# Kernel optimization log

Hardware: AMD Instinct MI355X
Metric: run time of the kernel (lower is better)

Reference implementation:

```python
import math
import jax, jax.numpy as jnp
import numpy as np

B, S, E, H = 1, 2048, 2048, 16
QL, KL = 1536, 512          # q_lora_rank, kv_lora_rank
DN, DR, DV = 128, 64, 128   # qk_nope_head_dim, qk_rope_head_dim, v_head_dim
DQ = DN + DR                # q_head_dim = 192
ROPE_BASE = 10000.0
EPS = 1e-6


def _rope_cache(seq_len):
    # YaRN with scaling_factor=1.0 reduces exactly to standard RoPE (freq_extra == freq_inter,
    # mscale ratio == 1), matching DeepseekV2YarnRotaryEmbedding at default settings.
    inv_freq = 1.0 / (ROPE_BASE ** (np.arange(0, DR, 2, dtype=np.float32) / DR))
    t = np.arange(seq_len, dtype=np.float32)
    freqs = np.outer(t, inv_freq)
    emb = np.concatenate([freqs, freqs], axis=-1)  # (S, DR)
    return jnp.asarray(np.cos(emb)), jnp.asarray(np.sin(emb))


def _rmsnorm(x, w):
    return x * jax.lax.rsqrt(jnp.mean(x * x, axis=-1, keepdims=True) + EPS) * w


def _apply_rope(x, cos, sin):
    # x: (B, S, H, D). DeepseekV2 apply_rotary_pos_emb first de-interleaves
    # (view(..., d//2, 2).transpose) then uses rotate_half.
    b, s, h, d = x.shape
    xr = x.reshape(b, s, h, d // 2, 2)
    x = jnp.concatenate([xr[..., 0], xr[..., 1]], axis=-1)  # de-interleave
    rot = jnp.concatenate([-x[..., d // 2:], x[..., : d // 2]], axis=-1)
    return x * cos[None, :, None, :] + rot * sin[None, :, None, :]


def setup_inputs() -> dict:
    key = jax.random.key(0)
    ks = jax.random.split(key, 8)
    w = lambda k, shape, fan_in: (jax.random.normal(k, shape, jnp.float32) / math.sqrt(fan_in))
    return {
        "x": jax.random.normal(ks[0], (B, S, E), jnp.float32),
        "w_q_a": w(ks[1], (E, QL), E),
        "q_a_ln": jnp.ones((QL,), jnp.float32),
        "w_q_b": w(ks[2], (QL, H * DQ), QL),
        "w_kv_a": w(ks[3], (E, KL + DR), E),
        "kv_a_ln": jnp.ones((KL,), jnp.float32),
        "w_kv_b": w(ks[4], (KL, H * (DN + DV)), KL),
        "w_out": w(ks[5], (H * DV, E), H * DV),
    }


def reference(x, w_q_a, q_a_ln, w_q_b, w_kv_a, kv_a_ln, w_kv_b, w_out):
    b, s, _ = x.shape
    # Q: low-rank down-proj -> RMSNorm -> up-proj, split nope/rope parts
    q = (_rmsnorm(x @ w_q_a, q_a_ln) @ w_q_b).reshape(b, s, H, DQ)
    q_nope, q_pe = q[..., :DN], q[..., DN:]
    # KV: joint compressed latent + shared (MQA-style) rope key
    ckv = x @ w_kv_a                         # (b, s, KL+DR)
    c_kv, k_pe = ckv[..., :KL], ckv[..., KL:]
    kv = (_rmsnorm(c_kv, kv_a_ln) @ w_kv_b).reshape(b, s, H, DN + DV)
    k_nope, v = kv[..., :DN], kv[..., DN:]
    # Partial RoPE on the 64-dim rope slice only
    cos, sin = _rope_cache(s)
    q_pe = _apply_rope(q_pe, cos, sin)
    k_pe = _apply_rope(k_pe.reshape(b, s, 1, DR), cos, sin)
    qf = jnp.concatenate([q_nope, q_pe], axis=-1)                       # (b,s,H,192)
    kf = jnp.concatenate([k_nope, jnp.broadcast_to(k_pe, (b, s, H, DR))], axis=-1)
    # Causal softmax attention, scale = 1/sqrt(q_head_dim)
    scale = 1.0 / math.sqrt(DQ)
    scores = jnp.einsum("bqhd,bkhd->bhqk", qf, kf) * scale
    mask = jnp.tril(jnp.ones((s, s), dtype=bool))
    scores = jnp.where(mask[None, None], scores, jnp.finfo(scores.dtype).min)
    p = jax.nn.softmax(scores, axis=-1)
    o = jnp.einsum("bhqk,bkhd->bqhd", p, v).reshape(b, s, H * DV)
    return o @ w_out
```

## Files before the change

### kernel.cpp

```cpp
#include <hip/hip_runtime.h>
#include <hip/hip_bf16.h>
#include <math.h>

#define SS   2048
#define EE   2048
#define HH   16
#define QLAT 1536
#define KLAT 512
#define DN   128
#define DR   64
#define DV   128
#define DQ   192
#define KVD  256
#define CKVW 576
#define QW   3072
#define KVW  4096
#define OW   2048
#define QAC  2112

#define NSEG 4
#define PT_STRIDE 72
#define KTSZ (6 * 64 * 32)

typedef __attribute__((ext_vector_type(8))) short short8;
typedef __attribute__((ext_vector_type(4))) float f32x4;

__global__ void detect_dtype(const unsigned int* __restrict__ lnw, int* flag) {
    *flag = (lnw[0] == 0x3F803F80u) ? 1 : 0;
}

__device__ __forceinline__ float ld_in(const void* p, size_t i, int bf) {
    if (bf) return __bfloat162float(((const __hip_bfloat16*)p)[i]);
    return ((const float*)p)[i];
}

__device__ __forceinline__ ushort f2b(float v) {
    __hip_bfloat16 b = __float2bfloat16(v);
    return *(ushort*)&b;
}
__device__ __forceinline__ float b2f(ushort u) {
    __hip_bfloat16 b = *(__hip_bfloat16*)&u;
    return __bfloat162float(b);
}

__device__ __forceinline__ void async16(const ushort* g, ushort* l) {
    __builtin_amdgcn_global_load_lds(
        (const __attribute__((address_space(1))) void*)g,
        (__attribute__((address_space(3))) void*)l, 16, 0, 0);
}

__global__ __launch_bounds__(256) void conv_x_bf(
    const void* __restrict__ src, ushort* __restrict__ dst, int n, const int* flag) {
    const int bf = *flag;
    int i = (blockIdx.x * 256 + threadIdx.x) * 4;
    if (i >= n) return;
    ushort4 u;
    u.x = f2b(ld_in(src, i + 0, bf));
    u.y = f2b(ld_in(src, i + 1, bf));
    u.z = f2b(ld_in(src, i + 2, bf));
    u.w = f2b(ld_in(src, i + 3, bf));
    *(ushort4*)(dst + i) = u;
}

__global__ __launch_bounds__(256) void transpose5_bf(
    const void* __restrict__ s0, const void* __restrict__ s1,
    const void* __restrict__ s2, const void* __restrict__ s3,
    const void* __restrict__ s4,
    ushort* __restrict__ d0, ushort* __restrict__ d1, ushort* __restrict__ d2,
    ushort* __restrict__ d3, ushort* __restrict__ d4,
    const int* flag) {
    const int z = blockIdx.z;
    const void* in; ushort* out; int R, C;
    switch (z) {
        case 0:  in = s0; out = d0; R = EE;   C = QLAT; break;
        case 1:  in = s1; out = d1; R = EE;   C = CKVW; break;
        case 2:  in = s2; out = d2; R = QLAT; C = QW;   break;
        case 3:  in = s3; out = d3; R = KLAT; C = KVW;  break;
        default: in = s4; out = d4; R = OW;   C = EE;   break;
    }
    const int c0 = blockIdx.x * 64, r0 = blockIdx.y * 64;
    if (c0 >= C || r0 >= R) return;
    const int bf = *flag;
    __shared__ ushort t[64][66];
    const int lane = threadIdx.x & 63, grp = threadIdx.x >> 6;
    #pragma unroll
    for (int p = 0; p < 16; ++p) {
        int r = p * 4 + grp;
        t[lane][r] = f2b(ld_in(in, (size_t)(r0 + r) * C + c0 + lane, bf));
    }
    __syncthreads();
    const int ro = (threadIdx.x & 31) * 2, co = threadIdx.x >> 5;
    #pragma unroll
    for (int p = 0; p < 8; ++p) {
        int c = p * 8 + co;
        ushort2 u = *(const ushort2*)&t[c][ro];
        *(ushort2*)&out[(size_t)(c0 + c) * R + r0 + ro] = u;
    }
}

__device__ __forceinline__ void gemm128_body(
    const ushort* __restrict__ A, const ushort* __restrict__ Bt,
    void* __restrict__ C, int N, int K, int lda, int ldb, int ldc,
    int cbf, int bm, int bn, ushort* As, ushort* Bs) {
    const int tid = threadIdx.x;
    const int lane = tid & 63, wv = tid >> 6;
    const int wm = (wv & 1) * 64, wn = (wv >> 1) * 64;
    const int ln = lane & 15, quad = lane >> 4;

    f32x4 acc[4][4];
    #pragma unroll
    for (int i = 0; i < 4; ++i)
        #pragma unroll
        for (int j = 0; j < 4; ++j) acc[i][j] = (f32x4){0.f, 0.f, 0.f, 0.f};

    const int srow = tid >> 3;
    const int spart = ((tid & 7) ^ ((tid >> 3) & 7)) * 8;
    const ushort* Ag0 = A + (size_t)(bm + srow) * lda + spart;
    const ushort* Ag1 = Ag0 + (size_t)32 * lda;
    const ushort* Ag2 = Ag0 + (size_t)64 * lda;
    const ushort* Ag3 = Ag0 + (size_t)96 * lda;
    const int br0 = (bn + srow)      < N ? (bn + srow)      : (N - 1);
    const int br1 = (bn + 32 + srow) < N ? (bn + 32 + srow) : (N - 1);
    const int br2 = (bn + 64 + srow) < N ? (bn + 64 + srow) : (N - 1);
    const int br3 = (bn + 96 + srow) < N ? (bn + 96 + srow) : (N - 1);
    const ushort* Bg0 = Bt + (size_t)br0 * ldb + spart;
    const ushort* Bg1 = Bt + (size_t)br1 * ldb + spart;
    const ushort* Bg2 = Bt + (size_t)br2 * ldb + spart;
    const ushort* Bg3 = Bt + (size_t)br3 * ldb + spart;
    const int nsteps = K >> 6;

    {
        ushort* as = As + tid * 8;
        ushort* bs = Bs + tid * 8;
        async16(Ag0, as);          async16(Ag1, as + 2048);
        async16(Ag2, as + 4096);   async16(Ag3, as + 6144);
        async16(Bg0, bs);          async16(Bg1, bs + 2048);
        async16(Bg2, bs + 4096);   async16(Bg3, bs + 6144);
    }

    int cb = 0;
    for (int c = 0; c < nsteps; ++c) {
        asm volatile("s_waitcnt vmcnt(0)" ::: "memory");
        __builtin_amdgcn_s_barrier();
        asm volatile("" ::: "memory");
        if (c + 1 < nsteps) {
            const int k1 = (c + 1) << 6;
            ushort* as = As + (cb ^ 1) * 8192 + tid * 8;
            ushort* bs = Bs + (cb ^ 1) * 8192 + tid * 8;
            async16(Ag0 + k1, as);          async16(Ag1 + k1, as + 2048);
            async16(Ag2 + k1, as + 4096);   async16(Ag3 + k1, as + 6144);
            async16(Bg0 + k1, bs);          async16(Bg1 + k1, bs + 2048);
            async16(Bg2 + k1, bs + 4096);   async16(Bg3 + k1, bs + 6144);
        }
        const ushort* Ac = As + cb * 8192;
        const ushort* Bc = Bs + cb * 8192;
        #pragma unroll
        for (int ks = 0; ks < 2; ++ks) {
            const int sw = ((ks * 4 + quad) ^ (ln & 7)) * 8;
            short8 af[4], bfr[4];
            #pragma unroll
            for (int t = 0; t < 4; ++t) {
                af[t]  = *(const short8*)&Ac[(wm + t * 16 + ln) * 64 + sw];
                bfr[t] = *(const short8*)&Bc[(wn + t * 16 + ln) * 64 + sw];
            }
            __builtin_amdgcn_s_setprio(1);
            #pragma unroll
            for (int i = 0; i < 4; ++i)
                #pragma unroll
                for (int j = 0; j < 4; ++j)
                    acc[i][j] = __builtin_amdgcn_mfma_f32_16x16x32_bf16(af[i], bfr[j], acc[i][j], 0, 0, 0);
            __builtin_amdgcn_s_setprio(0);
        }
        cb ^= 1;
    }

    #pragma unroll
    for (int i = 0; i < 4; ++i) {
        #pragma unroll
        for (int r = 0; r < 4; ++r) {
            const int m = bm + wm + i * 16 + quad * 4 + r;
            #pragma unroll
            for (int j = 0; j < 4; ++j) {
                const int n = bn + wn + j * 16 + ln;
                if (n < N) {
                    if (cbf) ((ushort*)C)[(size_t)m * ldc + n] = f2b(acc[i][j][r]);
                    else     ((float*)C)[(size_t)m * ldc + n] = acc[i][j][r];
                }
            }
        }
    }
}

__global__ __launch_bounds__(256) void gemm_qkv(
    const ushort* __restrict__ qac, const ushort* __restrict__ wqbt,
    const ushort* __restrict__ wkvbt, ushort* __restrict__ qbf_,
    ushort* __restrict__ kvbf_) {
    __shared__ ushort As[2 * 8192];
    __shared__ ushort Bs[2 * 8192];
    if (blockIdx.z == 0) {
        if (blockIdx.x >= QW / 128) return;
        gemm128_body(qac, wqbt, qbf_, QW, QLAT, QAC, QLAT, QW, 1,
                     blockIdx.y * 128, blockIdx.x * 128, As, Bs);
    } else {
        gemm128_body(qac + QLAT, wkvbt, kvbf_, KVW, KLAT, QAC, KLAT, KVW, 1,
                     blockIdx.y * 128, blockIdx.x * 128, As, Bs);
    }
}

__global__ __launch_bounds__(256) void gemm_bf64(
    const ushort* __restrict__ A, const ushort* __restrict__ Bt,
    void* __restrict__ C, int N, int K, int lda, int ldb, int ldc,
    int cmode, const int* __restrict__ cflag) {
    __shared__ ushort As[2 * 4096];
    __shared__ ushort Bs[2 * 8192];
    const int tid = threadIdx.x;
    const int bm = blockIdx.y * 64, bn = blockIdx.x * 128;
    const int lane = tid & 63, wv = tid >> 6;
    const int wm = (wv & 1) * 32, wn = (wv >> 1) * 64;
    const int ln = lane & 15, quad = lane >> 4;

    int cbf = cmode;
    if (cmode == 2) cbf = *(volatile const int*)cflag;

    f32x4 acc[2][4];
    #pragma unroll
    for (int i = 0; i < 2; ++i)
        #pragma unroll
        for (int j = 0; j < 4; ++j) acc[i][j] = (f32x4){0.f, 0.f, 0.f, 0.f};

    const int srow = tid >> 3;
    const int spart = ((tid & 7) ^ ((tid >> 3) & 7)) * 8;
    const ushort* Ag0 = A + (size_t)(bm + srow) * lda + spart;
    const ushort* Ag1 = Ag0 + (size_t)32 * lda;
    const int br0 = (bn + srow)      < N ? (bn + srow)      : (N - 1);
    const int br1 = (bn + 32 + srow) < N ? (bn + 32 + srow) : (N - 1);
    const int br2 = (bn + 64 + srow) < N ? (bn + 64 + srow) : (N - 1);
    const int br3 = (bn + 96 + srow) < N ? (bn + 96 + srow) : (N - 1);
    const ushort* Bg0 = Bt + (size_t)br0 * ldb + spart;
    const ushort* Bg1 = Bt + (size_t)br1 * ldb + spart;
    const ushort* Bg2 = Bt + (size_t)br2 * ldb + spart;
    const ushort* Bg3 = Bt + (size_t)br3 * ldb + spart;
    const int nsteps = K >> 6;

    {
        ushort* as = As + tid * 8;
        ushort* bs = Bs + tid * 8;
        async16(Ag0, as);          async16(Ag1, as + 2048);
        async16(Bg0, bs);          async16(Bg1, bs + 2048);
        async16(Bg2, bs + 4096);   async16(Bg3, bs + 6144);
    }

    int cb = 0;
    for (int c = 0; c < nsteps; ++c) {
        asm volatile("s_waitcnt vmcnt(0)" ::: "memory");
        __builtin_amdgcn_s_barrier();
        asm volatile("" ::: "memory");
        if (c + 1 < nsteps) {
            const int k1 = (c + 1) << 6;
            ushort* as = As + (cb ^ 1) * 4096 + tid * 8;
            ushort* bs = Bs + (cb ^ 1) * 8192 + tid * 8;
            async16(Ag0 + k1, as);          async16(Ag1 + k1, as + 2048);
            async16(Bg0 + k1, bs);          async16(Bg1 + k1, bs + 2048);
            async16(Bg2 + k1, bs + 4096);   async16(Bg3 + k1, bs + 6144);
        }
        const ushort* Ac = As + cb * 4096;
        const ushort* Bc = Bs + cb * 8192;
        #pragma unroll
        for (int ks = 0; ks < 2; ++ks) {
            const int sw = ((ks * 4 + quad) ^ (ln & 7)) * 8;
            short8 af[2], bfr[4];
            #pragma unroll
            for (int t = 0; t < 2; ++t)
                af[t] = *(const short8*)&Ac[(wm + t * 16 + ln) * 64 + sw];
            #pragma unroll
            for (int t = 0; t < 4; ++t)
                bfr[t] = *(const short8*)&Bc[(wn + t * 16 + ln) * 64 + sw];
            __builtin_amdgcn_s_setprio(1);
            #pragma unroll
            for (int i = 0; i < 2; ++i)
                #pragma unroll
                for (int j = 0; j < 4; ++j)
                    acc[i][j] = __builtin_amdgcn_mfma_f32_16x16x32_bf16(af[i], bfr[j], acc[i][j], 0, 0, 0);
            __builtin_amdgcn_s_setprio(0);
        }
        cb ^= 1;
    }

    #pragma unroll
    for (int i = 0; i < 2; ++i) {
        #pragma unroll
        for (int r = 0; r < 4; ++r) {
            const int m = bm + wm + i * 16 + quad * 4 + r;
            #pragma unroll
            for (int j = 0; j < 4; ++j) {
                const int n = bn + wn + j * 16 + ln;
                if (n < N) {
                    if (cbf) ((ushort*)C)[(size_t)m * ldc + n] = f2b(acc[i][j][r]);
                    else     ((float*)C)[(size_t)m * ldc + n] = acc[i][j][r];
                }
            }
        }
    }
}

__global__ __launch_bounds__(256) void rmsnorm2_bf(
    ushort* __restrict__ x, const void* __restrict__ wq,
    const void* __restrict__ wkv, const int* wflag) {
    const int wbf = *wflag;
    const int which = blockIdx.y;
    const int cols = which ? KLAT : QLAT;
    const void* w = which ? wkv : wq;
    ushort* p = x + (size_t)blockIdx.x * QAC + (which ? QLAT : 0);
    float ss = 0.f;
    for (int i = threadIdx.x; i < cols; i += 256) { float v = b2f(p[i]); ss += v * v; }
    #pragma unroll
    for (int off = 32; off; off >>= 1) ss += __shfl_xor(ss, off);
    __shared__ float red[4];
    const int wid = threadIdx.x >> 6, lane = threadIdx.x & 63;
    if (lane == 0) red[wid] = ss;
    __syncthreads();
    const float tot = red[0] + red[1] + red[2] + red[3];
    const float scale = rsqrtf(tot / (float)cols + 1e-6f);
    for (int i = threadIdx.x; i < cols; i += 256)
        p[i] = f2b(b2f(p[i]) * scale * ld_in(w, i, wbf));
}

__global__ __launch_bounds__(256) void rope_tab(float* __restrict__ tab) {
    int idx = blockIdx.x * 256 + threadIdx.x;
    int s = idx >> 5, i = idx & 31;
    float inv = powf(10000.0f, -(float)i / 32.0f);
    float sv, cv;
    sincosf((float)s * inv, &sv, &cv);
    tab[idx * 2]     = cv;
    tab[idx * 2 + 1] = sv;
}

__device__ __forceinline__ void rope_block(
    const ushort* __restrict__ src, ushort* __restrict__ dst,
    const float* __restrict__ tb) {
    short8 vin[8];
    #pragma unroll
    for (int t = 0; t < 8; ++t) vin[t] = *(const short8*)(src + t * 8);
    short8 lo[4], hi[4];
    #pragma unroll
    for (int t = 0; t < 4; ++t) {
        #pragma unroll
        for (int j = 0; j < 8; ++j) {
            const int i = t * 8 + j;
            float cv = tb[2 * i], sv = tb[2 * i + 1];
            ushort u0 = ((const ushort*)&vin[(2 * i) >> 3])[(2 * i) & 7];
            ushort u1 = ((const ushort*)&vin[(2 * i + 1) >> 3])[(2 * i + 1) & 7];
            float x0 = b2f(u0), x1 = b2f(u1);
            lo[t][j] = (short)f2b(x0 * cv - x1 * sv);
            hi[t][j] = (short)f2b(x1 * cv + x0 * sv);
        }
    }
    #pragma unroll
    for (int t = 0; t < 4; ++t) {
        *(short8*)(dst + t * 8)      = lo[t];
        *(short8*)(dst + 32 + t * 8) = hi[t];
    }
}

__global__ __launch_bounds__(256) void fuse3(
    ushort* __restrict__ q, const ushort* __restrict__ qac,
    const ushort* __restrict__ kv, ushort* __restrict__ kf,
    ushort* __restrict__ vt2, const float* __restrict__ tab) {
    __shared__ ushort Vl[64 * 136];
    const int b = blockIdx.x;
    const int tid = threadIdx.x;
    if (b < 128) {
        int idx = b * 256 + tid;
        int s = idx >> 4, h = idx & 15;
        ushort* p = q + (size_t)s * QW + h * DQ + DN;
        rope_block(p, p, tab + s * 64);
    } else if (b < 128 + 3072) {
        int idx = (b - 128) * 256 + tid;
        int part = idx % 24;
        int rest = idx / 24;
        int h = rest & 15, s = rest >> 4;
        short8 v;
        if (part < 16) {
            v = *(const short8*)(kv + (size_t)s * KVW + h * KVD + part * 8);
        } else {
            const int j8 = part - 16;
            const int seg = j8 & 3;
            const ushort* cp = qac + (size_t)s * QAC + QLAT + KLAT + seg * 16;
            short8 a = *(const short8*)cp;
            short8 bb = *(const short8*)(cp + 8);
            const float* tb = tab + s * 64 + seg * 16;
            const bool hi = (j8 >= 4);
            #pragma unroll
            for (int jj = 0; jj < 8; ++jj) {
                float cv = tb[2 * jj], sv = tb[2 * jj + 1];
                ushort u0 = (jj < 4) ? (ushort)a[2 * jj]     : (ushort)bb[2 * jj - 8];
                ushort u1 = (jj < 4) ? (ushort)a[2 * jj + 1] : (ushort)bb[2 * jj - 7];
                float x0 = b2f(u0), x1 = b2f(u1);
                v[jj] = (short)f2b(hi ? (x1 * cv + x0 * sv) : (x0 * cv - x1 * sv));
            }
        }
        *(short8*)(kf + ((size_t)h * SS + s) * 192 + part * 8) = v;
    } else {
        const int r = b - (128 + 3072);
        const int ck = r & 31, h = r >> 5;
        const int lane = tid & 63, wv = tid >> 6;
        #pragma unroll
        for (int rr = 0; rr < 4; ++rr) {
            int n = rr * 256 + tid;
            int key = n >> 4, part = n & 15;
            short8 v = *(const short8*)(kv + (size_t)(ck * 64 + key) * KVW + h * KVD + DN + part * 8);
            *(short8*)&Vl[key * 136 + part * 8] = v;
        }
        __syncthreads();
        const int ln = lane & 15, quad = lane >> 4;
        ushort* dst = vt2 + (((size_t)h * 32 + ck) * 16) * 512;
        #pragma unroll
        for (int w = 0; w < 4; ++w) {
            int idx2 = wv * 4 + w;
            int kb2 = idx2 >> 3, nb = idx2 & 7;
            short8 v;
            #pragma unroll
            for (int j = 0; j < 8; ++j)
                ((ushort*)&v)[j] = Vl[(kb2 * 32 + quad * 8 + j) * 136 + nb * 16 + ln];
            *(short8*)(dst + (size_t)idx2 * 512 + lane * 8) = v;
        }
    }
}

__global__ __launch_bounds__(256, 2) void attn_mfma2(
    const ushort* __restrict__ qbf, const ushort* __restrict__ kf,
    const ushort* __restrict__ vt2, ushort* __restrict__ opart,
    float* __restrict__ ml) {
    const int seg = blockIdx.x, bq = 31 - blockIdx.y, h = blockIdx.z;
    const int ctot = bq + 1;
    const int c_lo = (seg * ctot) >> 2;
    const int nch = (((seg + 1) * ctot) >> 2) - c_lo;
    if (nch <= 0) return;

    __shared__ ushort Kt[2 * KTSZ];
    __shared__ ushort Pt[4][16 * PT_STRIDE];

    const int tid = threadIdx.x, lane = tid & 63, wl = tid >> 6;
    const int ln = lane & 15, quad = lane >> 4;
    const int qw = bq * 64 + wl * 16;
    const int kstart = c_lo << 6;
    const float scale = 0.07216878364870322f;

    short8 aq[6];
    const ushort* qrow = qbf + (size_t)(qw + ln) * QW + h * DQ;
    #pragma unroll
    for (int kb = 0; kb < 6; ++kb)
        aq[kb] = *(const short8*)(qrow + kb * 32 + quad * 8);

    const ushort* kfh = kf + (size_t)h * SS * 192;
    const ushort* vth2 = vt2 + ((size_t)h * 32 * 16) * 512 + lane * 8;

    const int key_s = tid >> 2;
    const int swp = ((tid & 3) ^ ((tid >> 3) & 3)) * 8;
    const ushort* kg = kfh + (size_t)(kstart + key_s) * 192 + swp;
    const int swq = (quad ^ ((ln >> 1) & 3)) * 8;

    f32x4 oacc[8];
    #pragma unroll
    for (int f = 0; f < 8; ++f) oacc[f] = (f32x4){0.f, 0.f, 0.f, 0.f};
    float mrow[4] = {-INFINITY, -INFINITY, -INFINITY, -INFINITY};
    float lrow[4] = {0.f, 0.f, 0.f, 0.f};

    {
        ushort* kd = Kt + tid * 8;
        #pragma unroll
        for (int i = 0; i < 6; ++i)
            async16(kg + i * 32, kd + i * 2048);
        kg += (size_t)64 * 192;
    }

    for (int c = 0; c < nch; ++c) {
        const int k0 = kstart + (c << 6);
        asm volatile("s_waitcnt vmcnt(0)" ::: "memory");
        __builtin_amdgcn_s_barrier();
        asm volatile("" ::: "memory");
        if (c + 1 < nch) {
            ushort* kd = Kt + ((c + 1) & 1) * KTSZ + tid * 8;
            #pragma unroll
            for (int i = 0; i < 6; ++i)
                async16(kg + i * 32, kd + i * 2048);
            kg += (size_t)64 * 192;
        }
        const ushort* Kcur = Kt + (c & 1) * KTSZ;

        const ushort* vfr = vth2 + (size_t)(k0 >> 6) * 16 * 512;
        short8 bv0[8];
        #pragma unroll
        for (int nb = 0; nb < 8; ++nb)
            bv0[nb] = *(const short8*)(vfr + (size_t)nb * 512);
        f32x4 s[4];
        #pragma unroll
        for (int ns = 0; ns < 4; ++ns) s[ns] = (f32x4){0.f, 0.f, 0.f, 0.f};
        __builtin_amdgcn_s_setprio(1);
        #pragma unroll
        for (int ns = 0; ns < 4; ++ns)
            #pragma unroll
            for (int kb = 0; kb < 6; ++kb) {
                short8 bk = *(const short8*)&Kcur[(kb * 64 + ns * 16 + ln) * 32 + swq];
                s[ns] = __builtin_amdgcn_mfma_f32_16x16x32_bf16(aq[kb], bk, s[ns], 0, 0, 0);
            }
        __builtin_amdgcn_s_setprio(0);
        float pv[4][4], rmax[4];
        #pragma unroll
        for (int r = 0; r < 4; ++r) rmax[r] = -1e30f;
        #pragma unroll
        for (int ns = 0; ns < 4; ++ns)
            #pragma unroll
            for (int r = 0; r < 4; ++r) {
                int key = k0 + ns * 16 + ln;
                int qr = qw + quad * 4 + r;
                float v = s[ns][r] * scale;
                if (key > qr) v = -1e30f;
                pv[ns][r] = v;
                rmax[r] = fmaxf(rmax[r], v);
            }
        #pragma unroll
        for (int off = 8; off; off >>= 1)
            #pragma unroll
            for (int r = 0; r < 4; ++r)
                rmax[r] = fmaxf(rmax[r], __shfl_xor(rmax[r], off));
        float alpha[4], psum[4];
        #pragma unroll
        for (int r = 0; r < 4; ++r) {
            float mnew = fmaxf(mrow[r], rmax[r]);
            alpha[r] = __expf(mrow[r] - mnew);
            mrow[r] = mnew;
        }
        #pragma unroll
        for (int ns = 0; ns < 4; ++ns)
            #pragma unroll
            for (int r = 0; r < 4; ++r)
                pv[ns][r] = __expf(pv[ns][r] - mrow[r]);
        #pragma unroll
        for (int r = 0; r < 4; ++r)
            psum[r] = (pv[0][r] + pv[1][r]) + (pv[2][r] + pv[3][r]);
        #pragma unroll
        for (int off = 8; off; off >>= 1)
            #pragma unroll
            for (int r = 0; r < 4; ++r)
                psum[r] += __shfl_xor(psum[r], off);
        #pragma unroll
        for (int r = 0; r < 4; ++r) lrow[r] = lrow[r] * alpha[r] + psum[r];
        #pragma unroll
        for (int f = 0; f < 8; ++f)
            #pragma unroll
            for (int r = 0; r < 4; ++r) oacc[f][r] *= alpha[r];
        #pragma unroll
        for (int ns = 0; ns < 4; ++ns)
            #pragma unroll
            for (int r = 0; r < 4; ++r)
                Pt[wl][(quad * 4 + r) * PT_STRIDE + ns * 16 + ln] = f2b(pv[ns][r]);
        short8 bv1[8];
        #pragma unroll
        for (int nb = 0; nb < 8; ++nb)
            bv1[nb] = *(const short8*)(vfr + (size_t)(8 + nb) * 512);
        short8 pa0 = *(const short8*)&Pt[wl][ln * PT_STRIDE + quad * 8];
        short8 pa1 = *(const short8*)&Pt[wl][ln * PT_STRIDE + 32 + quad * 8];
        __builtin_amdgcn_s_setprio(1);
        #pragma unroll
        for (int nb = 0; nb < 8; ++nb)
            oacc[nb] = __builtin_amdgcn_mfma_f32_16x16x32_bf16(pa0, bv0[nb], oacc[nb], 0, 0, 0);
        #pragma unroll
        for (int nb = 0; nb < 8; ++nb)
            oacc[nb] = __builtin_amdgcn_mfma_f32_16x16x32_bf16(pa1, bv1[nb], oacc[nb], 0, 0, 0);
        __builtin_amdgcn_s_setprio(0);
    }

    const size_t pbase = (((size_t)h * 32 + bq) * NSEG + seg) * 64;
    #pragma unroll
    for (int nb = 0; nb < 8; ++nb)
        #pragma unroll
        for (int r = 0; r < 4; ++r)
            opart[(pbase + wl * 16 + quad * 4 + r) * 128 + nb * 16 + ln] = f2b(oacc[nb][r]);
    if (ln == 0) {
        #pragma unroll
        for (int r = 0; r < 4; ++r) {
            ml[(pbase + wl * 16 + quad * 4 + r) * 2]     = mrow[r];
            ml[(pbase + wl * 16 + quad * 4 + r) * 2 + 1] = lrow[r];
        }
    }
}

__global__ __launch_bounds__(256) void merge_attn(
    const ushort* __restrict__ opart, const float* __restrict__ ml,
    ushort* __restrict__ obf) {
    const int q = blockIdx.x;
    const int bq = q >> 6, row = q & 63;
    const int ctot = bq + 1;
    const int t = threadIdx.x;
    #pragma unroll
    for (int pp = 0; pp < 8; ++pp) {
        int idx = pp * 256 + t;
        int h = idx >> 7, d = idx & 127;
        size_t rbase = (((size_t)h * 32 + bq) * NSEG) * 64 + row;
        float M = -1e30f;
        #pragma unroll
        for (int s = 0; s < NSEG; ++s) {
            if ((((s + 1) * ctot) >> 2) > ((s * ctot) >> 2))
                M = fmaxf(M, ml[(rbase + (size_t)s * 64) * 2]);
        }
        float L = 0.f, acc = 0.f;
        #pragma unroll
        for (int s = 0; s < NSEG; ++s) {
            if ((((s + 1) * ctot) >> 2) > ((s * ctot) >> 2)) {
                size_t ri = rbase + (size_t)s * 64;
                float w = __expf(ml[ri * 2] - M);
                L += w * ml[ri * 2 + 1];
                acc += w * b2f(opart[ri * 128 + d]);
            }
        }
        obf[(size_t)q * OW + h * DV + d] = f2b(acc / L);
    }
}

extern "C" void kernel_launch(void* const* d_in, const int* in_sizes, int n_in,
                              void* d_out, int out_size, void* d_ws, size_t ws_size,
                              hipStream_t stream) {
    const void* x       = d_in[0];
    const void* w_q_a   = d_in[1];
    const void* q_a_ln  = d_in[2];
    const void* w_q_b   = d_in[3];
    const void* w_kv_a  = d_in[4];
    const void* kv_a_ln = d_in[5];
    const void* w_kv_b  = d_in[6];
    const void* w_out   = d_in[7];

    char* ws = (char*)d_ws;
    int*    flag  = (int*)ws;
    ushort* qbf   = (ushort*)(ws + 256);
    ushort* obf   = qbf   + (size_t)SS * QW;
    ushort* wqat  = obf   + (size_t)SS * OW;
    ushort* wkvat = wqat  + (size_t)QLAT * EE;
    ushort* wqbt  = wkvat + (size_t)CKVW * EE;
    ushort* wkvbt = wqbt  + (size_t)QW * QLAT;
    ushort* woutt = wkvbt + (size_t)KVW * KLAT;
    ushort* kf    = woutt + (size_t)EE * OW;
    ushort* vt2   = kf    + (size_t)HH * SS * 192;
    float*  ml    = (float*)(vt2 + (size_t)HH * SS * DV);
    ushort* qac   = (ushort*)(ml + (size_t)HH * 32 * NSEG * 64 * 2);
    ushort* xbf   = qac   + (size_t)SS * QAC;
    ushort* kvbf  = xbf   + (size_t)SS * EE;
    ushort* kpebf = kvbf  + (size_t)SS * KVW;
    float*  rtab  = (float*)(kpebf + (size_t)SS * DR);
    ushort* opart = qac;

    detect_dtype<<<1, 1, 0, stream>>>((const unsigned int*)q_a_ln, flag);
    rope_tab<<<SS * 32 / 256, 256, 0, stream>>>(rtab);

    conv_x_bf<<<(SS * EE / 4 + 255) / 256, 256, 0, stream>>>(x, xbf, SS * EE, flag);
    transpose5_bf<<<dim3(64, 32, 5), 256, 0, stream>>>(
        w_q_a, w_kv_a, w_q_b, w_kv_b, w_out,
        wqat, wkvat, wqbt, wkvbt, woutt, flag);

    gemm_bf64<<<dim3((QAC + 127) / 128, SS / 64), 256, 0, stream>>>(
        xbf, wqat, qac, QAC, EE, EE, EE, QAC, 1, nullptr);

    rmsnorm2_bf<<<dim3(SS, 2), 256, 0, stream>>>(qac, q_a_ln, kv_a_ln, flag);

    gemm_qkv<<<dim3(KVW / 128, SS / 128, 2), 256, 0, stream>>>(
        qac, wqbt, wkvbt, qbf, kvbf);

    fuse3<<<128 + 3072 + 512, 256, 0, stream>>>(qbf, qac, kvbf, kf, vt2, rtab);

    attn_mfma2<<<dim3(NSEG, SS / 64, HH), 256, 0, stream>>>(qbf, kf, vt2, opart, ml);
    merge_attn<<<SS, 256, 0, stream>>>(opart, ml, obf);

    gemm_bf64<<<dim3(EE / 128, SS / 64), 256, 0, stream>>>(
        obf, woutt, d_out, EE, OW, OW, OW, EE, 2, flag);
}
```

Measured before the change: 372.2 us.

## Double query rows per attention block to reuse K/V tiles across two groups

Each attention workgroup now handles 128 query rows instead of 64, with each wave owning two 16-row groups that share the same K tile in LDS and the same V fragments. This halves K tile loads and block count per head. Fully masked chunks for a group are skipped, and the causal mask is applied only on diagonal chunks. The cost is higher register pressure from doubled accumulators and Q fragments, which may hurt occupancy with launch bounds of 2, plus fewer blocks to fill the GPU.

```diff
diff --git a/kernel.cpp b/kernel.cpp
--- a/kernel.cpp
+++ b/kernel.cpp
@@ -431,8 +431,8 @@
     const ushort* __restrict__ qbf, const ushort* __restrict__ kf,
     const ushort* __restrict__ vt2, ushort* __restrict__ opart,
     float* __restrict__ ml) {
-    const int seg = blockIdx.x, bq = 31 - blockIdx.y, h = blockIdx.z;
-    const int ctot = bq + 1;
+    const int seg = blockIdx.x, bq = 15 - blockIdx.y, h = blockIdx.z;
+    const int ctot = 2 * bq + 2;
     const int c_lo = (seg * ctot) >> 2;
     const int nch = (((seg + 1) * ctot) >> 2) - c_lo;
     if (nch <= 0) return;
@@ -442,15 +442,18 @@
 
     const int tid = threadIdx.x, lane = tid & 63, wl = tid >> 6;
     const int ln = lane & 15, quad = lane >> 4;
-    const int qw = bq * 64 + wl * 16;
+    const int qw = bq * 128 + wl * 32;
     const int kstart = c_lo << 6;
     const float scale = 0.07216878364870322f;
 
-    short8 aq[6];
-    const ushort* qrow = qbf + (size_t)(qw + ln) * QW + h * DQ;
-    #pragma unroll
-    for (int kb = 0; kb < 6; ++kb)
-        aq[kb] = *(const short8*)(qrow + kb * 32 + quad * 8);
+    short8 aq[2][6];
+    #pragma unroll
+    for (int g = 0; g < 2; ++g) {
+        const ushort* qrow = qbf + (size_t)(qw + g * 16 + ln) * QW + h * DQ;
+        #pragma unroll
+        for (int kb = 0; kb < 6; ++kb)
+            aq[g][kb] = *(const short8*)(qrow + kb * 32 + quad * 8);
+    }
 
     const ushort* kfh = kf + (size_t)h * SS * 192;
     const ushort* vth2 = vt2 + ((size_t)h * 32 * 16) * 512 + lane * 8;
@@ -460,11 +463,16 @@
     const ushort* kg = kfh + (size_t)(kstart + key_s) * 192 + swp;
     const int swq = (quad ^ ((ln >> 1) & 3)) * 8;
 
-    f32x4 oacc[8];
-    #pragma unroll
-    for (int f = 0; f < 8; ++f) oacc[f] = (f32x4){0.f, 0.f, 0.f, 0.f};
-    float mrow[4] = {-INFINITY, -INFINITY, -INFINITY, -INFINITY};
-    float lrow[4] = {0.f, 0.f, 0.f, 0.f};
+    f32x4 oacc[2][8];
+    #pragma unroll
+    for (int g = 0; g < 2; ++g)
+        #pragma unroll
+        for (int f = 0; f < 8; ++f) oacc[g][f] = (f32x4){0.f, 0.f, 0.f, 0.f};
+    float mrow[2][4], lrow[2][4];
+    #pragma unroll
+    for (int g = 0; g < 2; ++g)
+        #pragma unroll
+        for (int r = 0; r < 4; ++r) { mrow[g][r] = -INFINITY; lrow[g][r] = 0.f; }
 
     {
         ushort* kd = Kt + tid * 8;
@@ -487,101 +495,112 @@
             kg += (size_t)64 * 192;
         }
         const ushort* Kcur = Kt + (c & 1) * KTSZ;
-
         const ushort* vfr = vth2 + (size_t)(k0 >> 6) * 16 * 512;
-        short8 bv0[8];
+
+        #pragma unroll
+        for (int g = 0; g < 2; ++g) {
+            const int qg = qw + g * 16;
+            if (k0 > qg + 15) continue;
+            f32x4 s[4];
+            #pragma unroll
+            for (int ns = 0; ns < 4; ++ns) s[ns] = (f32x4){0.f, 0.f, 0.f, 0.f};
+            __builtin_amdgcn_s_setprio(1);
+            #pragma unroll
+            for (int ns = 0; ns < 4; ++ns)
+                #pragma unroll
+                for (int kb = 0; kb < 6; ++kb) {
+                    short8 bk = *(const short8*)&Kcur[(kb * 64 + ns * 16 + ln) * 32 + swq];
+                    s[ns] = __builtin_amdgcn_mfma_f32_16x16x32_bf16(aq[g][kb], bk, s[ns], 0, 0, 0);
+                }
+            __builtin_amdgcn_s_setprio(0);
+            float pv[4][4], rmax[4];
+            #pragma unroll
+            for (int ns = 0; ns < 4; ++ns)
+                #pragma unroll
+                for (int r = 0; r < 4; ++r)
+                    pv[ns][r] = s[ns][r] * scale;
+            if (k0 + 63 > qg) {
+                #pragma unroll
+                for (int ns = 0; ns < 4; ++ns)
+                    #pragma unroll
+                    for (int r = 0; r < 4; ++r)
+                        if (k0 + ns * 16 + ln > qg + quad * 4 + r) pv[ns][r] = -1e30f;
+            }
+            #pragma unroll
+            for (int r = 0; r < 4; ++r)
+                rmax[r] = fmaxf(fmaxf(pv[0][r], pv[1][r]), fmaxf(pv[2][r], pv[3][r]));
+            #pragma unroll
+            for (int off = 8; off; off >>= 1)
+                #pragma unroll
+                for (int r = 0; r < 4; ++r)
+                    rmax[r] = fmaxf(rmax[r], __shfl_xor(rmax[r], off));
+            float alpha[4], psum[4];
+            #pragma unroll
+            for (int r = 0; r < 4; ++r) {
+                float mnew = fmaxf(mrow[g][r], rmax[r]);
+                alpha[r] = __expf(mrow[g][r] - mnew);
+                mrow[g][r] = mnew;
+            }
+            #pragma unroll
+            for (int ns = 0; ns < 4; ++ns)
+                #pragma unroll
+                for (int r = 0; r < 4; ++r)
+                    pv[ns][r] = __expf(pv[ns][r] - mrow[g][r]);
+            #pragma unroll
+            for (int r = 0; r < 4; ++r)
+                psum[r] = (pv[0][r] + pv[1][r]) + (pv[2][r] + pv[3][r]);
+            #pragma unroll
+            for (int off = 8; off; off >>= 1)
+                #pragma unroll
+                for (int r = 0; r < 4; ++r)
+                    psum[r] += __shfl_xor(psum[r], off);
+            #pragma unroll
+            for (int r = 0; r < 4; ++r) lrow[g][r] = lrow[g][r] * alpha[r] + psum[r];
+            #pragma unroll
+            for (int f = 0; f < 8; ++f)
+                #pragma unroll
+                for (int r = 0; r < 4; ++r) oacc[g][f][r] *= alpha[r];
+            #pragma unroll
+            for (int ns = 0; ns < 4; ++ns)
+                #pragma unroll
+                for (int r = 0; r < 4; ++r)
+                    Pt[wl][(quad * 4 + r) * PT_STRIDE + ns * 16 + ln] = f2b(pv[ns][r]);
+            short8 bv0[8], bv1[8];
+            #pragma unroll
+            for (int nb = 0; nb < 8; ++nb) {
+                bv0[nb] = *(const short8*)(vfr + (size_t)nb * 512);
+                bv1[nb] = *(const short8*)(vfr + (size_t)(8 + nb) * 512);
+            }
+            short8 pa0 = *(const short8*)&Pt[wl][ln * PT_STRIDE + quad * 8];
+            short8 pa1 = *(const short8*)&Pt[wl][ln * PT_STRIDE + 32 + quad * 8];
+            __builtin_amdgcn_s_setprio(1);
+            #pragma unroll
+            for (int nb = 0; nb < 8; ++nb)
+                oacc[g][nb] = __builtin_amdgcn_mfma_f32_16x16x32_bf16(pa0, bv0[nb], oacc[g][nb], 0, 0, 0);
+            #pragma unroll
+            for (int nb = 0; nb < 8; ++nb)
+                oacc[g][nb] = __builtin_amdgcn_mfma_f32_16x16x32_bf16(pa1, bv1[nb], oacc[g][nb], 0, 0, 0);
+            __builtin_amdgcn_s_setprio(0);
+        }
+    }
+
+    const size_t pbase = (((size_t)h * 16 + bq) * NSEG + seg) * 128;
+    #pragma unroll
+    for (int g = 0; g < 2; ++g) {
         #pragma unroll
         for (int nb = 0; nb < 8; ++nb)
-            bv0[nb] = *(const short8*)(vfr + (size_t)nb * 512);
-        f32x4 s[4];
-        #pragma unroll
-        for (int ns = 0; ns < 4; ++ns) s[ns] = (f32x4){0.f, 0.f, 0.f, 0.f};
-        __builtin_amdgcn_s_setprio(1);
-        #pragma unroll
-        for (int ns = 0; ns < 4; ++ns)
-            #pragma unroll
-            for (int kb = 0; kb < 6; ++kb) {
-                short8 bk = *(const short8*)&Kcur[(kb * 64 + ns * 16 + ln) * 32 + swq];
-                s[ns] = __builtin_amdgcn_mfma_f32_16x16x32_bf16(aq[kb], bk, s[ns], 0, 0, 0);
-            }
-        __builtin_amdgcn_s_setprio(0);
-        float pv[4][4], rmax[4];
-        #pragma unroll
-        for (int r = 0; r < 4; ++r) rmax[r] = -1e30f;
-        #pragma unroll
-        for (int ns = 0; ns < 4; ++ns)
             #pragma unroll
             for (int r = 0; r < 4; ++r) {
-                int key = k0 + ns * 16 + ln;
-                int qr = qw + quad * 4 + r;
-                float v = s[ns][r] * scale;
-                if (key > qr) v = -1e30f;
-                pv[ns][r] = v;
-                rmax[r] = fmaxf(rmax[r], v);
-            }
-        #pragma unroll
-        for (int off = 8; off; off >>= 1)
-            #pragma unroll
-            for (int r = 0; r < 4; ++r)
-                rmax[r] = fmaxf(rmax[r], __shfl_xor(rmax[r], off));
-        float alpha[4], psum[4];
-        #pragma unroll
-        for (int r = 0; r < 4; ++r) {
-            float mnew = fmaxf(mrow[r], rmax[r]);
-            alpha[r] = __expf(mrow[r] - mnew);
-            mrow[r] = mnew;
-        }
-        #pragma unroll
-        for (int ns = 0; ns < 4; ++ns)
-            #pragma unroll
-            for (int r = 0; r < 4; ++r)
-                pv[ns][r] = __expf(pv[ns][r] - mrow[r]);
-        #pragma unroll
-        for (int r = 0; r < 4; ++r)
-            psum[r] = (pv[0][r] + pv[1][r]) + (pv[2][r] + pv[3][r]);
-        #pragma unroll
-        for (int off = 8; off; off >>= 1)
-            #pragma unroll
-            for (int r = 0; r < 4; ++r)
-                psum[r] += __shfl_xor(psum[r], off);
-        #pragma unroll
-        for (int r = 0; r < 4; ++r) lrow[r] = lrow[r] * alpha[r] + psum[r];
-        #pragma unroll
-        for (int f = 0; f < 8; ++f)
-            #pragma unroll
-            for (int r = 0; r < 4; ++r) oacc[f][r] *= alpha[r];
-        #pragma unroll
-        for (int ns = 0; ns < 4; ++ns)
-            #pragma unroll
-            for (int r = 0; r < 4; ++r)
-                Pt[wl][(quad * 4 + r) * PT_STRIDE + ns * 16 + ln] = f2b(pv[ns][r]);
-        short8 bv1[8];
-        #pragma unroll
-        for (int nb = 0; nb < 8; ++nb)
-            bv1[nb] = *(const short8*)(vfr + (size_t)(8 + nb) * 512);
-        short8 pa0 = *(const short8*)&Pt[wl][ln * PT_STRIDE + quad * 8];
-        short8 pa1 = *(const short8*)&Pt[wl][ln * PT_STRIDE + 32 + quad * 8];
-        __builtin_amdgcn_s_setprio(1);
-        #pragma unroll
-        for (int nb = 0; nb < 8; ++nb)
-            oacc[nb] = __builtin_amdgcn_mfma_f32_16x16x32_bf16(pa0, bv0[nb], oacc[nb], 0, 0, 0);
-        #pragma unroll
-        for (int nb = 0; nb < 8; ++nb)
-            oacc[nb] = __builtin_amdgcn_mfma_f32_16x16x32_bf16(pa1, bv1[nb], oacc[nb], 0, 0, 0);
-        __builtin_amdgcn_s_setprio(0);
-    }
-
-    const size_t pbase = (((size_t)h * 32 + bq) * NSEG + seg) * 64;
-    #pragma unroll
-    for (int nb = 0; nb < 8; ++nb)
-        #pragma unroll
-        for (int r = 0; r < 4; ++r)
-            opart[(pbase + wl * 16 + quad * 4 + r) * 128 + nb * 16 + ln] = f2b(oacc[nb][r]);
-    if (ln == 0) {
-        #pragma unroll
-        for (int r = 0; r < 4; ++r) {
-            ml[(pbase + wl * 16 + quad * 4 + r) * 2]     = mrow[r];
-            ml[(pbase + wl * 16 + quad * 4 + r) * 2 + 1] = lrow[r];
+                const int row = wl * 32 + g * 16 + quad * 4 + r;
+                opart[(pbase + row) * 128 + nb * 16 + ln] = f2b(oacc[g][nb][r]);
+            }
+        if (ln == 0) {
+            #pragma unroll
+            for (int r = 0; r < 4; ++r) {
+                const int row = wl * 32 + g * 16 + quad * 4 + r;
+                ml[(pbase + row) * 2]     = mrow[g][r];
+                ml[(pbase + row) * 2 + 1] = lrow[g][r];
+            }
         }
     }
 }
@@ -590,25 +609,25 @@
     const ushort* __restrict__ opart, const float* __restrict__ ml,
     ushort* __restrict__ obf) {
     const int q = blockIdx.x;
-    const int bq = q >> 6, row = q & 63;
-    const int ctot = bq + 1;
+    const int bq = q >> 7, row = q & 127;
+    const int ctot = 2 * bq + 2;
     const int t = threadIdx.x;
     #pragma unroll
     for (int pp = 0; pp < 8; ++pp) {
         int idx = pp * 256 + t;
         int h = idx >> 7, d = idx & 127;
-        size_t rbase = (((size_t)h * 32 + bq) * NSEG) * 64 + row;
+        size_t rbase = (((size_t)h * 16 + bq) * NSEG) * 128 + row;
         float M = -1e30f;
         #pragma unroll
         for (int s = 0; s < NSEG; ++s) {
             if ((((s + 1) * ctot) >> 2) > ((s * ctot) >> 2))
-                M = fmaxf(M, ml[(rbase + (size_t)s * 64) * 2]);
+                M = fmaxf(M, ml[(rbase + (size_t)s * 128) * 2]);
         }
         float L = 0.f, acc = 0.f;
         #pragma unroll
         for (int s = 0; s < NSEG; ++s) {
             if ((((s + 1) * ctot) >> 2) > ((s * ctot) >> 2)) {
-                size_t ri = rbase + (size_t)s * 64;
+                size_t ri = rbase + (size_t)s * 128;
                 float w = __expf(ml[ri * 2] - M);
                 L += w * ml[ri * 2 + 1];
                 acc += w * b2f(opart[ri * 128 + d]);
@@ -642,7 +661,7 @@
     ushort* kf    = woutt + (size_t)EE * OW;
     ushort* vt2   = kf    + (size_t)HH * SS * 192;
     float*  ml    = (float*)(vt2 + (size_t)HH * SS * DV);
-    ushort* qac   = (ushort*)(ml + (size_t)HH * 32 * NSEG * 64 * 2);
+    ushort* qac   = (ushort*)(ml + (size_t)HH * 16 * NSEG * 128 * 2);
     ushort* xbf   = qac   + (size_t)SS * QAC;
     ushort* kvbf  = xbf   + (size_t)SS * EE;
     ushort* kpebf = kvbf  + (size_t)SS * KVW;
@@ -667,7 +686,7 @@
 
     fuse3<<<128 + 3072 + 512, 256, 0, stream>>>(qbf, qac, kvbf, kf, vt2, rtab);
 
-    attn_mfma2<<<dim3(NSEG, SS / 64, HH), 256, 0, stream>>>(qbf, kf, vt2, opart, ml);
+    attn_mfma2<<<dim3(NSEG, SS / 128, HH), 256, 0, stream>>>(qbf, kf, vt2, opart, ml);
     merge_attn<<<SS, 256, 0, stream>>>(opart, ml, obf);
 
     gemm_bf64<<<dim3(EE / 128, SS / 64), 256, 0, stream>>>(
```

After: 392.0 us. +5.3%, slower.
